# Performance work log

Measured on AMD Instinct MI355X. Metric: run time of the kernel, lower is better.

The kernel has to match this reference:

```python
import jax, jax.numpy as jnp
import numpy as np

N = 131072
N_DENSE, N_SPARSE, EMB = 13, 26, 16
N_FIELD = N_DENSE + N_SPARSE
VOCAB = 100000
HID = 32
EPS = 1e-5


def setup_inputs() -> dict:
    key = jax.random.key(0)
    ks = jax.random.split(key, 18)
    D = N_FIELD * EMB  # 624
    return {
        "Xi_dense": jax.random.normal(ks[0], (N, N_DENSE), jnp.float32),
        "Xi_sparse": jax.random.randint(ks[1], (N, N_SPARSE), 0, VOCAB),
        "Xv": jax.random.uniform(ks[2], (N, N_FIELD), dtype=jnp.float32),
        "bias": jax.random.normal(ks[3], (N,), jnp.float32),
        # first-order embeddings (13 Linear(1,E) + 26 Embedding tables)
        "W1d": jax.random.normal(ks[4], (N_DENSE, EMB), jnp.float32) * 0.1,
        "b1d": jax.random.normal(ks[5], (N_DENSE, EMB), jnp.float32) * 0.1,
        "T1": jax.random.normal(ks[6], (N_SPARSE, VOCAB, EMB), jnp.float32) * 0.1,
        # second-order embeddings
        "W2d": jax.random.normal(ks[7], (N_DENSE, EMB), jnp.float32) * 0.1,
        "b2d": jax.random.normal(ks[8], (N_DENSE, EMB), jnp.float32) * 0.1,
        "T2": jax.random.normal(ks[9], (N_SPARSE, VOCAB, EMB), jnp.float32) * 0.1,
        # deep MLP: 624 -> 32 -> 32, each layer followed by BatchNorm1d
        "Wl1": jax.random.normal(ks[10], (D, HID), jnp.float32) * (1.0 / np.sqrt(D)),
        "bl1": jax.random.normal(ks[11], (HID,), jnp.float32) * 0.1,
        "g1": jax.random.uniform(ks[12], (HID,), jnp.float32, 0.5, 1.5),
        "be1": jax.random.normal(ks[13], (HID,), jnp.float32) * 0.1,
        "Wl2": jax.random.normal(ks[14], (HID, HID), jnp.float32) * (1.0 / np.sqrt(HID)),
        "bl2": jax.random.normal(ks[15], (HID,), jnp.float32) * 0.1,
        "g2": jax.random.uniform(ks[16], (HID,), jnp.float32, 0.5, 1.5),
        "be2": jax.random.normal(ks[17], (HID,), jnp.float32) * 0.1,
    }


def _field_embed(Xi_dense, Xi_sparse, Xv, Wd, bd, T):
    # dense fields: Linear(1, E) per field -> (N, 13, E)
    dense = Xi_dense[:, :, None] * Wd[None] + bd[None]
    # sparse fields: per-field table gather -> (N, 26, E)
    sparse = T[jnp.arange(N_SPARSE)[None, :], Xi_sparse]
    emb = jnp.concatenate([dense, sparse], axis=1)  # (N, 39, E)
    return emb * Xv[:, :, None]


def _batchnorm(x, g, b):
    # BatchNorm1d in training mode: batch statistics, biased variance
    m = jnp.mean(x, axis=0)
    v = jnp.mean((x - m) ** 2, axis=0)
    return g * (x - m) * jax.lax.rsqrt(v + EPS) + b


def reference(Xi_dense, Xi_sparse, Xv, bias, W1d, b1d, T1, W2d, b2d, T2,
              Wl1, bl1, g1, be1, Wl2, bl2, g2, be2):
    first = _field_embed(Xi_dense, Xi_sparse, Xv, W1d, b1d, T1)   # (N, 39, E)
    second = _field_embed(Xi_dense, Xi_sparse, Xv, W2d, b2d, T2)  # (N, 39, E)

    # FM 2nd order: 0.5 * ((sum v)^2 - sum v^2)
    s = second.sum(axis=1)                                 # (N, E)
    fm2 = 0.5 * (s * s - (second * second).sum(axis=1))    # (N, E)

    # deep part on concatenated second-order field embeddings
    deep = second.reshape(second.shape[0], -1)             # (N, 39*E)
    h = _batchnorm(deep @ Wl1 + bl1, g1, be1)
    # dropout is identity at eval time
    h = _batchnorm(h @ Wl2 + bl2, g2, be2)

    total = first.sum(axis=(1, 2)) + fm2.sum(axis=1) + h.sum(axis=1) + bias
    return total
```

## Files before the change

### kernel.cpp

```cpp
#include <hip/hip_runtime.h>

#define NROWS  131072
#define ND     13
#define NS     26
#define NF     39
#define EMBD   16
#define DDIM   624
#define HIDN   32
#define VOCABN 100000
#define EPSF   1e-5f
#define NREP   64

__global__ __launch_bounds__(256, 3) void k1_embed(
    const float* __restrict__ Xi_dense, const int* __restrict__ Xi_sparse,
    const float* __restrict__ Xv, const float* __restrict__ bias,
    const float* __restrict__ W1d, const float* __restrict__ b1d,
    const float* __restrict__ T1,
    const float* __restrict__ W2d, const float* __restrict__ b2d,
    const float* __restrict__ T2,
    const float* __restrict__ Wl1, const float* __restrict__ bl1,
    float* __restrict__ base, float* __restrict__ y1,
    float* __restrict__ S1rep, float* __restrict__ Mrep)
{
    __shared__ float4 deep4[16 * 156];
    __shared__ float  xv_s[16 * NF];
    __shared__ int    xs_s[16 * NS];
    __shared__ float  xd_s[16 * ND];
    __shared__ float  sden[16][16];
    __shared__ float  ys[16][HIDN];

    const int t  = threadIdx.x;
    const int n0 = blockIdx.x * 16;

    for (int i = t; i < 16 * NF; i += 256) xv_s[i] = Xv[n0 * NF + i];
    for (int i = t; i < 16 * NS; i += 256) xs_s[i] = Xi_sparse[n0 * NS + i];
    for (int i = t; i < 16 * ND; i += 256) xd_s[i] = Xi_dense[n0 * ND + i];
    __syncthreads();

    const int r = t >> 4;
    const int q = t & 15;
    const int n = n0 + r;
    float* drow = (float*)deep4 + r * DDIM;

    const int pp = q & 3;
    const int p4 = pp * 4;
    const int fb = q >> 2;

    float4 A[7], B[7];
    float  xvv[7];
    #pragma unroll
    for (int i = 0; i < 7; ++i) {
        int  fs    = fb + 4 * i;
        bool valid = (fs < NS);
        int  fse   = valid ? fs : 0;
        xvv[i] = valid ? xv_s[r * NF + ND + fse] : 0.f;
        int ix  = xs_s[r * NS + fse];
        int off = (fse * VOCABN + ix) * EMBD + p4;
        A[i] = *(const float4*)(T1 + off);
        B[i] = *(const float4*)(T2 + off);
    }

    float first_p = 0.f, ssq_p = 0.f, sq = 0.f;
    #pragma unroll
    for (int f = 0; f < ND; ++f) {
        float xv = xv_s[r * NF + f];
        float xd = xd_s[r * ND + f];
        float v1 = fmaf(xd, W1d[f * EMBD + q], b1d[f * EMBD + q]) * xv;
        float v2 = fmaf(xd, W2d[f * EMBD + q], b2d[f * EMBD + q]) * xv;
        first_p += v1;
        sq += v2;
        ssq_p = fmaf(v2, v2, ssq_p);
        drow[f * EMBD + q] = v2;
    }
    sden[r][q] = sq;

    float4 s4 = make_float4(0.f, 0.f, 0.f, 0.f);
    #pragma unroll
    for (int i = 0; i < 7; ++i) {
        float  xv = xvv[i];
        float4 a  = A[i];
        float4 b  = B[i];
        first_p = fmaf(xv, (a.x + a.y) + (a.z + a.w), first_p);
        float4 v2 = make_float4(b.x * xv, b.y * xv, b.z * xv, b.w * xv);
        s4.x += v2.x; s4.y += v2.y; s4.z += v2.z; s4.w += v2.w;
        ssq_p = fmaf(v2.x, v2.x, ssq_p);
        ssq_p = fmaf(v2.y, v2.y, ssq_p);
        ssq_p = fmaf(v2.z, v2.z, ssq_p);
        ssq_p = fmaf(v2.w, v2.w, ssq_p);
        int fs = fb + 4 * i;
        if (fs < NS) deep4[r * 156 + (ND + fs) * 4 + pp] = v2;
    }

    s4.x += __shfl_xor(s4.x, 4, 64);  s4.y += __shfl_xor(s4.y, 4, 64);
    s4.z += __shfl_xor(s4.z, 4, 64);  s4.w += __shfl_xor(s4.w, 4, 64);
    s4.x += __shfl_xor(s4.x, 8, 64);  s4.y += __shfl_xor(s4.y, 8, 64);
    s4.z += __shfl_xor(s4.z, 8, 64);  s4.w += __shfl_xor(s4.w, 8, 64);

    __syncthreads();

    float4 sd = *(const float4*)(&sden[r][p4]);
    float sx = s4.x + sd.x, sy = s4.y + sd.y, sz = s4.z + sd.z, sw = s4.w + sd.w;
    float sdot = sx * sx + sy * sy + sz * sz + sw * sw;
    float contrib = first_p - 0.5f * ssq_p + ((q < 4) ? 0.5f * sdot : 0.f);
    contrib += __shfl_xor(contrib, 1, 64);
    contrib += __shfl_xor(contrib, 2, 64);
    contrib += __shfl_xor(contrib, 4, 64);
    contrib += __shfl_xor(contrib, 8, 64);
    if (q == 0) base[n] = contrib + bias[n];

    const int ds  = t & 15;
    const int cB  = ((t >> 6) & 1) * 4 + ((t >> 4) & 3);
    const int rgB = t >> 7;
    const float4* __restrict__ Wv4 = (const float4*)Wl1;
    const float4* arow = deep4 + (rgB * 8) * 156;

    float4 acc[8];
    #pragma unroll
    for (int rr = 0; rr < 8; ++rr) acc[rr] = make_float4(0.f, 0.f, 0.f, 0.f);

    #pragma unroll 3
    for (int k = 0; k < 9; ++k) {
        const int ch = ds + 16 * k;
        const int dbase = (4 * ch) * 8 + cB;
        float4 w0 = Wv4[dbase];
        float4 w1 = Wv4[dbase + 8];
        float4 w2 = Wv4[dbase + 16];
        float4 w3 = Wv4[dbase + 24];
        #pragma unroll
        for (int rr = 0; rr < 8; ++rr) {
            float4 a = arow[rr * 156 + ch];
            acc[rr].x = fmaf(a.x, w0.x, acc[rr].x); acc[rr].y = fmaf(a.x, w0.y, acc[rr].y);
            acc[rr].z = fmaf(a.x, w0.z, acc[rr].z); acc[rr].w = fmaf(a.x, w0.w, acc[rr].w);
            acc[rr].x = fmaf(a.y, w1.x, acc[rr].x); acc[rr].y = fmaf(a.y, w1.y, acc[rr].y);
            acc[rr].z = fmaf(a.y, w1.z, acc[rr].z); acc[rr].w = fmaf(a.y, w1.w, acc[rr].w);
            acc[rr].x = fmaf(a.z, w2.x, acc[rr].x); acc[rr].y = fmaf(a.z, w2.y, acc[rr].y);
            acc[rr].z = fmaf(a.z, w2.z, acc[rr].z); acc[rr].w = fmaf(a.z, w2.w, acc[rr].w);
            acc[rr].x = fmaf(a.w, w3.x, acc[rr].x); acc[rr].y = fmaf(a.w, w3.y, acc[rr].y);
            acc[rr].z = fmaf(a.w, w3.z, acc[rr].z); acc[rr].w = fmaf(a.w, w3.w, acc[rr].w);
        }
    }
    if (ds < 12) {
        const int ch = ds + 144;
        const int dbase = (4 * ch) * 8 + cB;
        float4 w0 = Wv4[dbase];
        float4 w1 = Wv4[dbase + 8];
        float4 w2 = Wv4[dbase + 16];
        float4 w3 = Wv4[dbase + 24];
        #pragma unroll
        for (int rr = 0; rr < 8; ++rr) {
            float4 a = arow[rr * 156 + ch];
            acc[rr].x = fmaf(a.x, w0.x, acc[rr].x); acc[rr].y = fmaf(a.x, w0.y, acc[rr].y);
            acc[rr].z = fmaf(a.x, w0.z, acc[rr].z); acc[rr].w = fmaf(a.x, w0.w, acc[rr].w);
            acc[rr].x = fmaf(a.y, w1.x, acc[rr].x); acc[rr].y = fmaf(a.y, w1.y, acc[rr].y);
            acc[rr].z = fmaf(a.y, w1.z, acc[rr].z); acc[rr].w = fmaf(a.y, w1.w, acc[rr].w);
            acc[rr].x = fmaf(a.z, w2.x, acc[rr].x); acc[rr].y = fmaf(a.z, w2.y, acc[rr].y);
            acc[rr].z = fmaf(a.z, w2.z, acc[rr].z); acc[rr].w = fmaf(a.z, w2.w, acc[rr].w);
            acc[rr].x = fmaf(a.w, w3.x, acc[rr].x); acc[rr].y = fmaf(a.w, w3.y, acc[rr].y);
            acc[rr].z = fmaf(a.w, w3.z, acc[rr].z); acc[rr].w = fmaf(a.w, w3.w, acc[rr].w);
        }
    }

    #pragma unroll
    for (int rr = 0; rr < 8; ++rr) {
        #pragma unroll
        for (int m = 1; m <= 8; m <<= 1) {
            acc[rr].x += __shfl_xor(acc[rr].x, m, 64);
            acc[rr].y += __shfl_xor(acc[rr].y, m, 64);
            acc[rr].z += __shfl_xor(acc[rr].z, m, 64);
            acc[rr].w += __shfl_xor(acc[rr].w, m, 64);
        }
    }

    if (ds == 0) {
        float4 bv = ((const float4*)bl1)[cB];
        #pragma unroll
        for (int rr = 0; rr < 8; ++rr) {
            const int row = rgB * 8 + rr;
            float4 v = acc[rr];
            v.x += bv.x; v.y += bv.y; v.z += bv.z; v.w += bv.w;
            ((float4*)(y1 + (size_t)(n0 + row) * HIDN))[cB] = v;
            *(float4*)&ys[row][4 * cB] = v;
        }
    }
    __syncthreads();

    const int rep = blockIdx.x & (NREP - 1);
    if (t < HIDN) {
        float s = 0.f;
        #pragma unroll
        for (int rr = 0; rr < 16; ++rr) s += ys[rr][t];
        atomicAdd(&S1rep[rep * HIDN + t], s);
    }
    {
        const int j1 = t >> 3;
        const int qd = t & 7;
        float4 mp = make_float4(0.f, 0.f, 0.f, 0.f);
        #pragma unroll
        for (int rr = 0; rr < 16; ++rr) {
            float  a1 = ys[rr][j1];
            float4 b4 = *(const float4*)&ys[rr][qd * 4];
            mp.x = fmaf(a1, b4.x, mp.x);
            mp.y = fmaf(a1, b4.y, mp.y);
            mp.z = fmaf(a1, b4.z, mp.z);
            mp.w = fmaf(a1, b4.w, mp.w);
        }
        float* Md = &Mrep[rep * 1024 + t * 4];
        atomicAdd(Md + 0, mp.x);
        atomicAdd(Md + 1, mp.y);
        atomicAdd(Md + 2, mp.z);
        atomicAdd(Md + 3, mp.w);
    }
}

__global__ void k2_post(const float* __restrict__ S1rep, const float* __restrict__ Mrep,
                        const float* __restrict__ g1, const float* __restrict__ be1,
                        const float* __restrict__ Wl2, const float* __restrict__ bl2,
                        const float* __restrict__ g2, const float* __restrict__ be2,
                        float* __restrict__ wvec, float* __restrict__ Cc)
{
    __shared__ float Ms[1024], Vs[1024];
    __shared__ float S1s[HIDN], alpha[HIDN], beta[HIDN], cv[HIDN];
    __shared__ float gam[HIDN], cpart[HIDN];
    __shared__ float qpart[8][HIDN];
    const int t = threadIdx.x;

    {
        float4 a4 = make_float4(0.f, 0.f, 0.f, 0.f);
        for (int rep = 0; rep < NREP; ++rep) {
            float4 v = ((const float4*)(Mrep + rep * 1024))[t];
            a4.x += v.x; a4.y += v.y; a4.z += v.z; a4.w += v.w;
        }
        ((float4*)Ms)[t] = a4;
    }
    if (t < HIDN) {
        float s = 0.f;
        for (int rep = 0; rep < NREP; ++rep) s += S1rep[rep * HIDN + t];
        S1s[t] = s;
    }
    __syncthreads();
    if (t < HIDN) {
        float m   = S1s[t] * (1.f / NROWS);
        float var = Ms[t * HIDN + t] * (1.f / NROWS) - m * m;
        float a   = g1[t] * rsqrtf(var + EPSF);
        alpha[t] = a;
        beta[t]  = be1[t] - a * m;
    }
    __syncthreads();
    for (int i = 0; i < 4; ++i) {
        int idx = t + 256 * i;
        Vs[idx] = alpha[idx >> 5] * Wl2[idx];
    }
    if (t < HIDN) {
        float c = bl2[t];
        for (int k = 0; k < HIDN; ++k) c = fmaf(beta[k], Wl2[k * HIDN + t], c);
        cv[t] = c;
    }
    __syncthreads();
    {
        const int j = t & 31, kg = t >> 5;
        float qp = 0.f;
        for (int kk = 0; kk < 4; ++kk) {
            int k = kg * 4 + kk;
            float u = 0.f;
            #pragma unroll
            for (int l = 0; l < HIDN; ++l) u = fmaf(Ms[k * HIDN + l], Vs[l * HIDN + j], u);
            qp = fmaf(Vs[k * HIDN + j], u, qp);
        }
        qpart[kg][j] = qp;
    }
    __syncthreads();
    if (t < HIDN) {
        float vmv = 0.f;
        #pragma unroll
        for (int g = 0; g < 8; ++g) vmv += qpart[g][t];
        float sv = 0.f;
        #pragma unroll
        for (int k = 0; k < HIDN; ++k) sv = fmaf(S1s[k], Vs[k * HIDN + t], sv);
        float S2 = sv + (float)NROWS * cv[t];
        float Q2 = vmv + 2.f * cv[t] * sv + (float)NROWS * cv[t] * cv[t];
        float m2 = S2 * (1.f / NROWS);
        float v2 = Q2 * (1.f / NROWS) - m2 * m2;
        float g  = g2[t] * rsqrtf(v2 + EPSF);
        gam[t]   = g;
        cpart[t] = g * (cv[t] - m2) + be2[t];
    }
    __syncthreads();
    if (t < HIDN) {
        float w = 0.f;
        #pragma unroll
        for (int j = 0; j < HIDN; ++j) w = fmaf(gam[j], Vs[t * HIDN + j], w);
        wvec[t] = w;
    }
    if (t == 0) {
        float C = 0.f;
        #pragma unroll
        for (int j = 0; j < HIDN; ++j) C += cpart[j];
        Cc[0] = C;
    }
}

__global__ __launch_bounds__(256) void k5_final(
    const float* __restrict__ y1, const float* __restrict__ base,
    const float* __restrict__ wvec, const float* __restrict__ Cc,
    float* __restrict__ out)
{
    __shared__ float ws_s[HIDN];
    __shared__ float Cs;
    const int t = threadIdx.x;
    if (t < HIDN) ws_s[t] = wvec[t];
    if (t == 0) Cs = Cc[0];
    __syncthreads();
    const size_t n = (size_t)blockIdx.x * 256 + t;
    const float4* yv = (const float4*)(y1 + n * HIDN);
    float acc = base[n] + Cs;
    #pragma unroll
    for (int kk = 0; kk < 8; ++kk) {
        float4 v = yv[kk];
        acc = fmaf(v.x, ws_s[4 * kk + 0], acc);
        acc = fmaf(v.y, ws_s[4 * kk + 1], acc);
        acc = fmaf(v.z, ws_s[4 * kk + 2], acc);
        acc = fmaf(v.w, ws_s[4 * kk + 3], acc);
    }
    out[n] = acc;
}

extern "C" void kernel_launch(void* const* d_in, const int* in_sizes, int n_in,
                              void* d_out, int out_size, void* d_ws, size_t ws_size,
                              hipStream_t stream)
{
    const float* Xi_dense = (const float*)d_in[0];
    const int*   Xi_sparse= (const int*)  d_in[1];
    const float* Xv       = (const float*)d_in[2];
    const float* bias     = (const float*)d_in[3];
    const float* W1d      = (const float*)d_in[4];
    const float* b1d      = (const float*)d_in[5];
    const float* T1       = (const float*)d_in[6];
    const float* W2d      = (const float*)d_in[7];
    const float* b2d      = (const float*)d_in[8];
    const float* T2       = (const float*)d_in[9];
    const float* Wl1      = (const float*)d_in[10];
    const float* bl1      = (const float*)d_in[11];
    const float* g1       = (const float*)d_in[12];
    const float* be1      = (const float*)d_in[13];
    const float* Wl2      = (const float*)d_in[14];
    const float* bl2      = (const float*)d_in[15];
    const float* g2       = (const float*)d_in[16];
    const float* be2      = (const float*)d_in[17];
    float* out = (float*)d_out;

    float* ws    = (float*)d_ws;
    float* S1rep = ws + 0;
    float* Mrep  = ws + 2048;
    float* wvec  = ws + 67584;
    float* Cc    = ws + 67616;
    float* base  = ws + 67840;
    float* y1    = ws + 198912;

    hipMemsetAsync(ws, 0, 67584 * sizeof(float), stream);

    k1_embed<<<NROWS / 16, 256, 0, stream>>>(Xi_dense, Xi_sparse, Xv, bias,
                                             W1d, b1d, T1, W2d, b2d, T2,
                                             Wl1, bl1, base, y1, S1rep, Mrep);
    k2_post<<<1, 256, 0, stream>>>(S1rep, Mrep, g1, be1, Wl2, bl2, g2, be2,
                                   wvec, Cc);
    k5_final<<<NROWS / 256, 256, 0, stream>>>(y1, base, wvec, Cc, out);
}
```

Baseline: 592.7 us.

## Make embed kernel persistent with LDS-resident Wl1 and prefetched gathers

Turns k1_embed into a persistent kernel with 256 blocks. Each block walks 32 row tiles, stages the whole swizzled Wl1 matrix once in LDS, and keeps the dense-field weights in registers. It prefetches the next tile's indices and embedding gathers while the current tile's GEMV runs, and it accumulates the BN statistics in registers so atomics are issued once per block. The aim is to hide gather latency and remove repeated Wl1 global reads. In exchange it uses only 256 blocks with occupancy 1, roughly 100KB of LDS, and heavy register pressure, which may leave many CUs idle or underused.

```diff
diff --git a/kernel.cpp b/kernel.cpp
--- a/kernel.cpp
+++ b/kernel.cpp
@@ -10,8 +10,45 @@
 #define VOCABN 100000
 #define EPSF   1e-5f
 #define NREP   64
-
-__global__ __launch_bounds__(256, 3) void k1_embed(
+#define NTILES (NROWS / 16)
+#define GRIDK1 256
+#define TPBT   (NTILES / GRIDK1)
+
+__device__ __forceinline__ void block_sync_lds() {
+    asm volatile("s_waitcnt lgkmcnt(0)" ::: "memory");
+    __builtin_amdgcn_s_barrier();
+    __builtin_amdgcn_sched_barrier(0);
+}
+
+__device__ __forceinline__ void fma16(float4& acc, const float4 a,
+                                      const float4 w0, const float4 w1,
+                                      const float4 w2, const float4 w3)
+{
+    acc.x = fmaf(a.x, w0.x, acc.x); acc.y = fmaf(a.x, w0.y, acc.y);
+    acc.z = fmaf(a.x, w0.z, acc.z); acc.w = fmaf(a.x, w0.w, acc.w);
+    acc.x = fmaf(a.y, w1.x, acc.x); acc.y = fmaf(a.y, w1.y, acc.y);
+    acc.z = fmaf(a.y, w1.z, acc.z); acc.w = fmaf(a.y, w1.w, acc.w);
+    acc.x = fmaf(a.z, w2.x, acc.x); acc.y = fmaf(a.z, w2.y, acc.y);
+    acc.z = fmaf(a.z, w2.z, acc.z); acc.w = fmaf(a.z, w2.w, acc.w);
+    acc.x = fmaf(a.w, w3.x, acc.x); acc.y = fmaf(a.w, w3.y, acc.y);
+    acc.z = fmaf(a.w, w3.z, acc.z); acc.w = fmaf(a.w, w3.w, acc.w);
+}
+
+#define PHASEB_CHUNK(CH) {                                              \
+    const int d0_ = (CH) << 2;                                          \
+    const int sw_ = ((CH) & 1) << 2;                                    \
+    float4 w0 = Wlds[(d0_    ) * 8 + (cB ^ (sw_ | 0))];                 \
+    float4 w1 = Wlds[(d0_ + 1) * 8 + (cB ^ (sw_ | 1))];                 \
+    float4 w2 = Wlds[(d0_ + 2) * 8 + (cB ^ (sw_ | 2))];                 \
+    float4 w3 = Wlds[(d0_ + 3) * 8 + (cB ^ (sw_ | 3))];                 \
+    _Pragma("unroll")                                                   \
+    for (int rr = 0; rr < 8; ++rr) {                                    \
+        float4 a = deep4[(rgB * 8 + rr) * 156 + (CH)];                  \
+        fma16(acc[rr], a, w0, w1, w2, w3);                              \
+    }                                                                   \
+}
+
+__global__ __launch_bounds__(256, 1) void k1_embed(
     const float* __restrict__ Xi_dense, const int* __restrict__ Xi_sparse,
     const float* __restrict__ Xv, const float* __restrict__ bias,
     const float* __restrict__ W1d, const float* __restrict__ b1d,
@@ -22,193 +59,206 @@
     float* __restrict__ base, float* __restrict__ y1,
     float* __restrict__ S1rep, float* __restrict__ Mrep)
 {
+    __shared__ float4 Wlds[DDIM * 8];
     __shared__ float4 deep4[16 * 156];
-    __shared__ float  xv_s[16 * NF];
-    __shared__ int    xs_s[16 * NS];
-    __shared__ float  xd_s[16 * ND];
-    __shared__ float  sden[16][16];
     __shared__ float  ys[16][HIDN];
 
     const int t  = threadIdx.x;
-    const int n0 = blockIdx.x * 16;
-
-    for (int i = t; i < 16 * NF; i += 256) xv_s[i] = Xv[n0 * NF + i];
-    for (int i = t; i < 16 * NS; i += 256) xs_s[i] = Xi_sparse[n0 * NS + i];
-    for (int i = t; i < 16 * ND; i += 256) xd_s[i] = Xi_dense[n0 * ND + i];
-    __syncthreads();
-
-    const int r = t >> 4;
-    const int q = t & 15;
-    const int n = n0 + r;
-    float* drow = (float*)deep4 + r * DDIM;
-
+    const int r  = t >> 4;
+    const int q  = t & 15;
     const int pp = q & 3;
     const int p4 = pp * 4;
     const int fb = q >> 2;
 
-    float4 A[7], B[7];
-    float  xvv[7];
-    #pragma unroll
-    for (int i = 0; i < 7; ++i) {
-        int  fs    = fb + 4 * i;
-        bool valid = (fs < NS);
-        int  fse   = valid ? fs : 0;
-        xvv[i] = valid ? xv_s[r * NF + ND + fse] : 0.f;
-        int ix  = xs_s[r * NS + fse];
-        int off = (fse * VOCABN + ix) * EMBD + p4;
-        A[i] = *(const float4*)(T1 + off);
-        B[i] = *(const float4*)(T2 + off);
-    }
-
-    float first_p = 0.f, ssq_p = 0.f, sq = 0.f;
-    #pragma unroll
-    for (int f = 0; f < ND; ++f) {
-        float xv = xv_s[r * NF + f];
-        float xd = xd_s[r * ND + f];
-        float v1 = fmaf(xd, W1d[f * EMBD + q], b1d[f * EMBD + q]) * xv;
-        float v2 = fmaf(xd, W2d[f * EMBD + q], b2d[f * EMBD + q]) * xv;
-        first_p += v1;
-        sq += v2;
-        ssq_p = fmaf(v2, v2, ssq_p);
-        drow[f * EMBD + q] = v2;
-    }
-    sden[r][q] = sq;
-
-    float4 s4 = make_float4(0.f, 0.f, 0.f, 0.f);
-    #pragma unroll
-    for (int i = 0; i < 7; ++i) {
-        float  xv = xvv[i];
-        float4 a  = A[i];
-        float4 b  = B[i];
-        first_p = fmaf(xv, (a.x + a.y) + (a.z + a.w), first_p);
-        float4 v2 = make_float4(b.x * xv, b.y * xv, b.z * xv, b.w * xv);
-        s4.x += v2.x; s4.y += v2.y; s4.z += v2.z; s4.w += v2.w;
-        ssq_p = fmaf(v2.x, v2.x, ssq_p);
-        ssq_p = fmaf(v2.y, v2.y, ssq_p);
-        ssq_p = fmaf(v2.z, v2.z, ssq_p);
-        ssq_p = fmaf(v2.w, v2.w, ssq_p);
-        int fs = fb + 4 * i;
-        if (fs < NS) deep4[r * 156 + (ND + fs) * 4 + pp] = v2;
-    }
-
-    s4.x += __shfl_xor(s4.x, 4, 64);  s4.y += __shfl_xor(s4.y, 4, 64);
-    s4.z += __shfl_xor(s4.z, 4, 64);  s4.w += __shfl_xor(s4.w, 4, 64);
-    s4.x += __shfl_xor(s4.x, 8, 64);  s4.y += __shfl_xor(s4.y, 8, 64);
-    s4.z += __shfl_xor(s4.z, 8, 64);  s4.w += __shfl_xor(s4.w, 8, 64);
-
-    __syncthreads();
-
-    float4 sd = *(const float4*)(&sden[r][p4]);
-    float sx = s4.x + sd.x, sy = s4.y + sd.y, sz = s4.z + sd.z, sw = s4.w + sd.w;
-    float sdot = sx * sx + sy * sy + sz * sz + sw * sw;
-    float contrib = first_p - 0.5f * ssq_p + ((q < 4) ? 0.5f * sdot : 0.f);
-    contrib += __shfl_xor(contrib, 1, 64);
-    contrib += __shfl_xor(contrib, 2, 64);
-    contrib += __shfl_xor(contrib, 4, 64);
-    contrib += __shfl_xor(contrib, 8, 64);
-    if (q == 0) base[n] = contrib + bias[n];
-
     const int ds  = t & 15;
     const int cB  = ((t >> 6) & 1) * 4 + ((t >> 4) & 3);
     const int rgB = t >> 7;
-    const float4* __restrict__ Wv4 = (const float4*)Wl1;
-    const float4* arow = deep4 + (rgB * 8) * 156;
-
-    float4 acc[8];
+
+    for (int i = t; i < DDIM * 8; i += 256) {
+        int d = i >> 3, c = i & 7;
+        Wlds[(d << 3) | (c ^ (d & 7))] = ((const float4*)Wl1)[i];
+    }
+
+    float w1r[ND], b1r[ND], w2r[ND], b2r[ND];
     #pragma unroll
-    for (int rr = 0; rr < 8; ++rr) acc[rr] = make_float4(0.f, 0.f, 0.f, 0.f);
-
-    #pragma unroll 3
-    for (int k = 0; k < 9; ++k) {
-        const int ch = ds + 16 * k;
-        const int dbase = (4 * ch) * 8 + cB;
-        float4 w0 = Wv4[dbase];
-        float4 w1 = Wv4[dbase + 8];
-        float4 w2 = Wv4[dbase + 16];
-        float4 w3 = Wv4[dbase + 24];
+    for (int f = 0; f < ND; ++f) {
+        w1r[f] = W1d[f * EMBD + q]; b1r[f] = b1d[f * EMBD + q];
+        w2r[f] = W2d[f * EMBD + q]; b2r[f] = b2d[f * EMBD + q];
+    }
+    const float4 blv = ((const float4*)bl1)[cB];
+
+    float4 mpA = make_float4(0.f, 0.f, 0.f, 0.f);
+    float  s1A = 0.f;
+    const int j1 = t >> 3, qd = t & 7;
+
+    float xdv[ND], xvd[ND], xvs[7], biasr;
+    int   idxr[7];
+    float4 A[7], B[7];
+
+    int tile = blockIdx.x;
+    {
+        const int n = tile * 16 + r;
+        const int*   xsp = Xi_sparse + n * NS;
+        const float* xvp = Xv + n * NF;
+        const float* xdp = Xi_dense + n * ND;
+        #pragma unroll
+        for (int i2 = 0; i2 < 7; ++i2) {
+            int fs = fb + 4 * i2; int fse = (fs < NS) ? fs : 0;
+            idxr[i2] = xsp[fse];
+            xvs[i2]  = (fs < NS) ? xvp[ND + fse] : 0.f;
+        }
+        #pragma unroll
+        for (int f = 0; f < ND; ++f) { xdv[f] = xdp[f]; xvd[f] = xvp[f]; }
+        biasr = bias[n];
+    }
+    block_sync_lds();
+    #pragma unroll
+    for (int i2 = 0; i2 < 7; ++i2) {
+        int fs = fb + 4 * i2; int fse = (fs < NS) ? fs : 0;
+        int off = (fse * VOCABN + idxr[i2]) * EMBD + p4;
+        A[i2] = *(const float4*)(T1 + off);
+        B[i2] = *(const float4*)(T2 + off);
+    }
+    __builtin_amdgcn_sched_barrier(0);
+
+    for (int it = 0; it < TPBT; ++it, tile += GRIDK1) {
+        const int n = tile * 16 + r;
+        float* drow = (float*)deep4 + r * DDIM;
+
+        float first_p = 0.f, ssq_p = 0.f, sq = 0.f;
+        #pragma unroll
+        for (int f = 0; f < ND; ++f) {
+            float xv = xvd[f], xd = xdv[f];
+            float v1 = fmaf(xd, w1r[f], b1r[f]) * xv;
+            float v2 = fmaf(xd, w2r[f], b2r[f]) * xv;
+            first_p += v1; sq += v2; ssq_p = fmaf(v2, v2, ssq_p);
+            drow[f * EMBD + q] = v2;
+        }
+        const int lb = t & 48;
+        float sdx = __shfl(sq, lb | (p4 + 0), 64);
+        float sdy = __shfl(sq, lb | (p4 + 1), 64);
+        float sdz = __shfl(sq, lb | (p4 + 2), 64);
+        float sdw = __shfl(sq, lb | (p4 + 3), 64);
+
+        float4 s4 = make_float4(0.f, 0.f, 0.f, 0.f);
+        #pragma unroll
+        for (int i2 = 0; i2 < 7; ++i2) {
+            float  xv = xvs[i2];
+            float4 a  = A[i2];
+            float4 b  = B[i2];
+            first_p = fmaf(xv, (a.x + a.y) + (a.z + a.w), first_p);
+            float4 v2 = make_float4(b.x * xv, b.y * xv, b.z * xv, b.w * xv);
+            s4.x += v2.x; s4.y += v2.y; s4.z += v2.z; s4.w += v2.w;
+            ssq_p = fmaf(v2.x, v2.x, ssq_p);
+            ssq_p = fmaf(v2.y, v2.y, ssq_p);
+            ssq_p = fmaf(v2.z, v2.z, ssq_p);
+            ssq_p = fmaf(v2.w, v2.w, ssq_p);
+            int fs = fb + 4 * i2;
+            if (fs < NS) deep4[r * 156 + (ND + fs) * 4 + pp] = v2;
+        }
+        s4.x += __shfl_xor(s4.x, 4, 64);  s4.y += __shfl_xor(s4.y, 4, 64);
+        s4.z += __shfl_xor(s4.z, 4, 64);  s4.w += __shfl_xor(s4.w, 4, 64);
+        s4.x += __shfl_xor(s4.x, 8, 64);  s4.y += __shfl_xor(s4.y, 8, 64);
+        s4.z += __shfl_xor(s4.z, 8, 64);  s4.w += __shfl_xor(s4.w, 8, 64);
+
+        float sx = s4.x + sdx, sy = s4.y + sdy, sz = s4.z + sdz, sw = s4.w + sdw;
+        float sdot = sx * sx + sy * sy + sz * sz + sw * sw;
+        float contrib = first_p - 0.5f * ssq_p + ((q < 4) ? 0.5f * sdot : 0.f);
+        contrib += __shfl_xor(contrib, 1, 64);
+        contrib += __shfl_xor(contrib, 2, 64);
+        contrib += __shfl_xor(contrib, 4, 64);
+        contrib += __shfl_xor(contrib, 8, 64);
+        if (q == 0) base[n] = contrib + biasr;
+
+        const bool hasNext = (it + 1 < TPBT);
+        if (hasNext) {
+            const int n2 = (tile + GRIDK1) * 16 + r;
+            const int*   xsp = Xi_sparse + n2 * NS;
+            const float* xvp = Xv + n2 * NF;
+            const float* xdp = Xi_dense + n2 * ND;
+            #pragma unroll
+            for (int i2 = 0; i2 < 7; ++i2) {
+                int fs = fb + 4 * i2; int fse = (fs < NS) ? fs : 0;
+                idxr[i2] = xsp[fse];
+                xvs[i2]  = (fs < NS) ? xvp[ND + fse] : 0.f;
+            }
+            #pragma unroll
+            for (int f = 0; f < ND; ++f) { xdv[f] = xdp[f]; xvd[f] = xvp[f]; }
+            biasr = bias[n2];
+        }
+
+        block_sync_lds();
+
+        if (hasNext) {
+            #pragma unroll
+            for (int i2 = 0; i2 < 7; ++i2) {
+                int fs = fb + 4 * i2; int fse = (fs < NS) ? fs : 0;
+                int off = (fse * VOCABN + idxr[i2]) * EMBD + p4;
+                A[i2] = *(const float4*)(T1 + off);
+                B[i2] = *(const float4*)(T2 + off);
+            }
+        }
+        __builtin_amdgcn_sched_barrier(0);
+
+        float4 acc[8];
+        #pragma unroll
+        for (int rr = 0; rr < 8; ++rr) acc[rr] = make_float4(0.f, 0.f, 0.f, 0.f);
+
+        #pragma unroll 3
+        for (int k = 0; k < 9; ++k) {
+            const int ch = ds + 16 * k;
+            PHASEB_CHUNK(ch)
+        }
+        if (ds < 12) {
+            const int ch = ds + 144;
+            PHASEB_CHUNK(ch)
+        }
+
         #pragma unroll
         for (int rr = 0; rr < 8; ++rr) {
-            float4 a = arow[rr * 156 + ch];
-            acc[rr].x = fmaf(a.x, w0.x, acc[rr].x); acc[rr].y = fmaf(a.x, w0.y, acc[rr].y);
-            acc[rr].z = fmaf(a.x, w0.z, acc[rr].z); acc[rr].w = fmaf(a.x, w0.w, acc[rr].w);
-            acc[rr].x = fmaf(a.y, w1.x, acc[rr].x); acc[rr].y = fmaf(a.y, w1.y, acc[rr].y);
-            acc[rr].z = fmaf(a.y, w1.z, acc[rr].z); acc[rr].w = fmaf(a.y, w1.w, acc[rr].w);
-            acc[rr].x = fmaf(a.z, w2.x, acc[rr].x); acc[rr].y = fmaf(a.z, w2.y, acc[rr].y);
-            acc[rr].z = fmaf(a.z, w2.z, acc[rr].z); acc[rr].w = fmaf(a.z, w2.w, acc[rr].w);
-            acc[rr].x = fmaf(a.w, w3.x, acc[rr].x); acc[rr].y = fmaf(a.w, w3.y, acc[rr].y);
-            acc[rr].z = fmaf(a.w, w3.z, acc[rr].z); acc[rr].w = fmaf(a.w, w3.w, acc[rr].w);
-        }
-    }
-    if (ds < 12) {
-        const int ch = ds + 144;
-        const int dbase = (4 * ch) * 8 + cB;
-        float4 w0 = Wv4[dbase];
-        float4 w1 = Wv4[dbase + 8];
-        float4 w2 = Wv4[dbase + 16];
-        float4 w3 = Wv4[dbase + 24];
-        #pragma unroll
-        for (int rr = 0; rr < 8; ++rr) {
-            float4 a = arow[rr * 156 + ch];
-            acc[rr].x = fmaf(a.x, w0.x, acc[rr].x); acc[rr].y = fmaf(a.x, w0.y, acc[rr].y);
-            acc[rr].z = fmaf(a.x, w0.z, acc[rr].z); acc[rr].w = fmaf(a.x, w0.w, acc[rr].w);
-            acc[rr].x = fmaf(a.y, w1.x, acc[rr].x); acc[rr].y = fmaf(a.y, w1.y, acc[rr].y);
-            acc[rr].z = fmaf(a.y, w1.z, acc[rr].z); acc[rr].w = fmaf(a.y, w1.w, acc[rr].w);
-            acc[rr].x = fmaf(a.z, w2.x, acc[rr].x); acc[rr].y = fmaf(a.z, w2.y, acc[rr].y);
-            acc[rr].z = fmaf(a.z, w2.z, acc[rr].z); acc[rr].w = fmaf(a.z, w2.w, acc[rr].w);
-            acc[rr].x = fmaf(a.w, w3.x, acc[rr].x); acc[rr].y = fmaf(a.w, w3.y, acc[rr].y);
-            acc[rr].z = fmaf(a.w, w3.z, acc[rr].z); acc[rr].w = fmaf(a.w, w3.w, acc[rr].w);
-        }
-    }
-
-    #pragma unroll
-    for (int rr = 0; rr < 8; ++rr) {
-        #pragma unroll
-        for (int m = 1; m <= 8; m <<= 1) {
-            acc[rr].x += __shfl_xor(acc[rr].x, m, 64);
-            acc[rr].y += __shfl_xor(acc[rr].y, m, 64);
-            acc[rr].z += __shfl_xor(acc[rr].z, m, 64);
-            acc[rr].w += __shfl_xor(acc[rr].w, m, 64);
-        }
-    }
-
-    if (ds == 0) {
-        float4 bv = ((const float4*)bl1)[cB];
-        #pragma unroll
-        for (int rr = 0; rr < 8; ++rr) {
-            const int row = rgB * 8 + rr;
-            float4 v = acc[rr];
-            v.x += bv.x; v.y += bv.y; v.z += bv.z; v.w += bv.w;
-            ((float4*)(y1 + (size_t)(n0 + row) * HIDN))[cB] = v;
-            *(float4*)&ys[row][4 * cB] = v;
-        }
-    }
-    __syncthreads();
-
-    const int rep = blockIdx.x & (NREP - 1);
-    if (t < HIDN) {
-        float s = 0.f;
-        #pragma unroll
-        for (int rr = 0; rr < 16; ++rr) s += ys[rr][t];
-        atomicAdd(&S1rep[rep * HIDN + t], s);
-    }
-    {
-        const int j1 = t >> 3;
-        const int qd = t & 7;
-        float4 mp = make_float4(0.f, 0.f, 0.f, 0.f);
+            #pragma unroll
+            for (int m = 1; m <= 8; m <<= 1) {
+                acc[rr].x += __shfl_xor(acc[rr].x, m, 64);
+                acc[rr].y += __shfl_xor(acc[rr].y, m, 64);
+                acc[rr].z += __shfl_xor(acc[rr].z, m, 64);
+                acc[rr].w += __shfl_xor(acc[rr].w, m, 64);
+            }
+        }
+        if (ds == 0) {
+            #pragma unroll
+            for (int rr = 0; rr < 8; ++rr) {
+                const int row = rgB * 8 + rr;
+                float4 v = acc[rr];
+                v.x += blv.x; v.y += blv.y; v.z += blv.z; v.w += blv.w;
+                ((float4*)(y1 + (size_t)(tile * 16 + row) * HIDN))[cB] = v;
+                *(float4*)&ys[row][4 * cB] = v;
+            }
+        }
+        block_sync_lds();
+
+        if (t < HIDN) {
+            #pragma unroll
+            for (int rr = 0; rr < 16; ++rr) s1A += ys[rr][t];
+        }
         #pragma unroll
         for (int rr = 0; rr < 16; ++rr) {
             float  a1 = ys[rr][j1];
             float4 b4 = *(const float4*)&ys[rr][qd * 4];
-            mp.x = fmaf(a1, b4.x, mp.x);
-            mp.y = fmaf(a1, b4.y, mp.y);
-            mp.z = fmaf(a1, b4.z, mp.z);
-            mp.w = fmaf(a1, b4.w, mp.w);
-        }
+            mpA.x = fmaf(a1, b4.x, mpA.x);
+            mpA.y = fmaf(a1, b4.y, mpA.y);
+            mpA.z = fmaf(a1, b4.z, mpA.z);
+            mpA.w = fmaf(a1, b4.w, mpA.w);
+        }
+    }
+
+    const int rep = blockIdx.x & (NREP - 1);
+    if (t < HIDN) atomicAdd(&S1rep[rep * HIDN + t], s1A);
+    {
         float* Md = &Mrep[rep * 1024 + t * 4];
-        atomicAdd(Md + 0, mp.x);
-        atomicAdd(Md + 1, mp.y);
-        atomicAdd(Md + 2, mp.z);
-        atomicAdd(Md + 3, mp.w);
+        atomicAdd(Md + 0, mpA.x);
+        atomicAdd(Md + 1, mpA.y);
+        atomicAdd(Md + 2, mpA.z);
+        atomicAdd(Md + 3, mpA.w);
     }
 }
 
@@ -358,9 +408,9 @@
 
     hipMemsetAsync(ws, 0, 67584 * sizeof(float), stream);
 
-    k1_embed<<<NROWS / 16, 256, 0, stream>>>(Xi_dense, Xi_sparse, Xv, bias,
-                                             W1d, b1d, T1, W2d, b2d, T2,
-                                             Wl1, bl1, base, y1, S1rep, Mrep);
+    k1_embed<<<GRIDK1, 256, 0, stream>>>(Xi_dense, Xi_sparse, Xv, bias,
+                                         W1d, b1d, T1, W2d, b2d, T2,
+                                         Wl1, bl1, base, y1, S1rep, Mrep);
     k2_post<<<1, 256, 0, stream>>>(S1rep, Mrep, g1, be1, Wl2, bl2, g2, be2,
                                    wvec, Cc);
     k5_final<<<NROWS / 256, 256, 0, stream>>>(y1, base, wvec, Cc, out);
```

Result: faster. 545.2 us (-8.0%).
